# Kernel optimization log

Measured on AMD Instinct MI355X. Metric: run time of the kernel, lower is better.

Reference implementation:

```python
import jax, jax.numpy as jnp
import numpy as np

N = 16
FS = 48000
NFFT = FS * 8            # irfft length hard-coded in the module
F = NFFT // 2 + 1        # 192001 frequency sample points
DELAYS = [809, 877, 937, 1049, 1151, 1249, 1373, 1499,
          1617, 1753, 1879, 2003, 2131, 2269, 2393, 2521]
GAIN_PER_SAMPLE = 0.9998


def setup_inputs() -> dict:
    key = jax.random.key(0)
    k1, k2, k3 = jax.random.split(key, 3)
    # frequency sample points on the upper half of the unit circle (rfft bins)
    omega = jnp.linspace(0.0, np.pi, F).astype(jnp.float32)
    x_real = jnp.cos(omega)
    x_imag = jnp.sin(omega)
    B = jax.random.normal(k1, (1, N, 1), dtype=jnp.float32) / N
    C = jax.random.normal(k2, (1, 1, N), dtype=jnp.float32) / N
    X = jax.random.normal(k3, (N, N), dtype=jnp.float32)  # raw Linear weight (pre-parametrization)
    return {"x_real": x_real, "x_imag": x_imag, "B": B, "C": C, "X": X}


def _delays_m():
    # torch does (m - mean)/std then forward undoes it: m = m_norm*std + mean
    m = jnp.asarray(DELAYS, dtype=jnp.float32)
    mStd = jnp.std(m, ddof=1)   # torch.std is unbiased
    mAvr = jnp.mean(m)
    m_norm = (m - mAvr) / mStd
    return m_norm * mStd + mAvr


def reference(x_real, x_imag, B, C, X):
    x = (x_real + 1j * x_imag).astype(jnp.complex64)          # [F]
    # Skew -> matrix_exp parametrization: A = expm(triu(X,1) - triu(X,1)^T), orthogonal
    Au = jnp.triu(X, 1)
    A = jax.scipy.linalg.expm(Au - Au.T)                       # [N, N]
    m = _delays_m()                                            # [N] float delays
    gamma = jnp.asarray(GAIN_PER_SAMPLE, jnp.float32) ** m     # diag of Gamma, [N]
    AG = (A * gamma[None, :]).astype(jnp.complex64)            # A @ diag(gamma), [N, N]
    # D = diag_embed(x[:,None] ** m) ; build (D - A Gamma) fused
    Dd = x[:, None] ** m[None, :]                              # [F, N] complex
    M = Dd[:, :, None] * jnp.eye(N, dtype=jnp.complex64) - AG[None, :, :]  # [F, N, N]
    Bc = B.astype(jnp.complex64)                               # [1, N, 1], broadcasts over F
    Hch = jnp.linalg.solve(M, Bc)                              # [F, N, 1]  == inv(M) @ B
    H = Hch[:, :, 0] * C.astype(jnp.complex64).reshape(1, N)   # [F, N]
    Hs = jnp.sum(H, axis=-1)                                   # [F]
    mask = jnp.where(x == 0, 0.0, 1.0).astype(jnp.complex64)   # H_mask zeroing x==0 bins
    h = jnp.fft.irfft(Hs * mask, n=NFFT)                       # [NFFT] real
    h = h / jnp.max(jnp.abs(h))
    return H, h
```

## Files before the change

### kernel.cpp

```cpp
#include <hip/hip_runtime.h>
#include <math.h>

#define NN 16
#define FF 192001
#define NFFTN 384000
#define N1F 1024
#define N2F 375
#define TWO_PI 6.283185307179586476925286766559

__constant__ float c_delays[16] = {809.f, 877.f, 937.f, 1049.f, 1151.f, 1249.f, 1373.f, 1499.f,
                                   1617.f, 1753.f, 1879.f, 2003.f, 2131.f, 2269.f, 2393.f, 2521.f};
__constant__ int c_idelays[16] = {809, 877, 937, 1049, 1151, 1249, 1373, 1499,
                                  1617, 1753, 1879, 2003, 2131, 2269, 2393, 2521};

typedef float v2f __attribute__((ext_vector_type(2)));

__device__ __forceinline__ float fastrcp(float x) {
#if __has_builtin(__builtin_amdgcn_rcpf)
  return __builtin_amdgcn_rcpf(x);
#else
  return 1.0f / x;
#endif
}

__global__ void expm_kernel(const float* __restrict__ X, float* __restrict__ AGout,
                            unsigned* __restrict__ mx) {
  if (threadIdx.x == 0) *mx = 0u;
  __shared__ double S[16][16], P[16][16], E[16][16];
  const int i = threadIdx.x >> 4, j = threadIdx.x & 15;
  double xu = (j > i) ? (double)X[i * 16 + j] : 0.0;
  double xl = (i > j) ? (double)X[j * 16 + i] : 0.0;
  double s = (xu - xl) * (1.0 / 256.0);
  S[i][j] = s;
  P[i][j] = s;
  E[i][j] = (i == j ? 1.0 : 0.0) + s;
  __syncthreads();
  for (int k = 2; k <= 24; ++k) {
    double acc = 0.0;
#pragma unroll
    for (int l = 0; l < 16; ++l) acc += P[i][l] * S[l][j];
    acc /= (double)k;
    __syncthreads();
    P[i][j] = acc;
    E[i][j] += acc;
    __syncthreads();
  }
  for (int t = 0; t < 8; ++t) {
    double acc = 0.0;
#pragma unroll
    for (int l = 0; l < 16; ++l) acc += E[i][l] * E[l][j];
    __syncthreads();
    E[i][j] = acc;
    __syncthreads();
  }
  double g = exp((double)c_delays[j] * log(0.9998));
  AGout[i * 16 + j] = (float)(E[i][j] * g);
}

template <int S>
__device__ __forceinline__ v2f bc8(v2f v) {
  v2f o;
  o[0] = __int_as_float(__builtin_amdgcn_ds_swizzle(__float_as_int(v[0]), (S << 5) | 0x18));
  o[1] = __int_as_float(__builtin_amdgcn_ds_swizzle(__float_as_int(v[1]), (S << 5) | 0x18));
  return o;
}

template <int K, int C>
struct ColLoop {
  static __device__ __forceinline__ void run(v2f (&A)[17], v2f (&B)[17],
                                             v2f nA0, v2f A1, v2f nB0, v2f B1) {
    v2f pc;
    if constexpr (K & 1) pc = bc8<(K >> 1)>(B[C]);
    else                 pc = bc8<(K >> 1)>(A[C]);
    v2f pcs = {pc[1], pc[0]};
    A[C] = __builtin_elementwise_fma(nA0, pc, A[C]);
    A[C] = __builtin_elementwise_fma(A1, pcs, A[C]);
    B[C] = __builtin_elementwise_fma(nB0, pc, B[C]);
    B[C] = __builtin_elementwise_fma(B1, pcs, B[C]);
    ColLoop<K, C + 1>::run(A, B, nA0, A1, nB0, B1);
  }
};
template <int K>
struct ColLoop<K, 17> {
  static __device__ __forceinline__ void run(v2f (&)[17], v2f (&)[17], v2f, v2f, v2f, v2f) {}
};

template <int K>
struct GJStep8 {
  static __device__ __forceinline__ void run(v2f (&A)[17], v2f (&B)[17], int s) {
    constexpr int S = K >> 1;
    v2f pk;
    if constexpr (K & 1) pk = bc8<S>(B[K]);
    else                 pk = bc8<S>(A[K]);
    float invd = fastrcp(pk[0] * pk[0] + pk[1] * pk[1]);
    float rcx = pk[0] * invd, rcy = -pk[1] * invd;
    bool ispA, ispB;
    if constexpr (K & 1) { ispA = false; ispB = (s == S); }
    else                 { ispA = (s == S); ispB = false; }
    v2f mA = A[K], mB = B[K];
    float frAx = ispA ? (1.0f - rcx) : (mA[0] * rcx - mA[1] * rcy);
    float frAy = ispA ? (-rcy)       : (mA[0] * rcy + mA[1] * rcx);
    float frBx = ispB ? (1.0f - rcx) : (mB[0] * rcx - mB[1] * rcy);
    float frBy = ispB ? (-rcy)       : (mB[0] * rcy + mB[1] * rcx);
    v2f nA0 = {-frAx, -frAx}, A1 = {frAy, -frAy};
    v2f nB0 = {-frBx, -frBx}, B1 = {frBy, -frBy};
    ColLoop<K, K + 1>::run(A, B, nA0, A1, nB0, B1);
    GJStep8<K + 1>::run(A, B, s);
  }
};
template <>
struct GJStep8<16> {
  static __device__ __forceinline__ void run(v2f (&)[17], v2f (&)[17], int) {}
};

template <bool CPLX>
__global__ __launch_bounds__(256, 4) void solve_kernel(
    const float* __restrict__ Bv, const float* __restrict__ Cv,
    const float* __restrict__ AGin, float* __restrict__ Hout,
    float2* __restrict__ G) {
  __shared__ float AGp[16][17];
  __shared__ float Bs[16], Cs[16];
  const int tid = threadIdx.x;
  AGp[tid >> 4][tid & 15] = AGin[tid];
  if (tid < 16) { Bs[tid] = Bv[tid]; Cs[tid] = Cv[tid]; }
  const int s = tid & 7;
  const int a = 2 * s, b = a + 1;
  int f = blockIdx.x * 32 + (tid >> 3);
  const bool active = (f < FF);
  if (!active) f = FF - 1;
  __syncthreads();

  int pa = (c_idelays[a] * f) % NFFTN;
  int pb = (c_idelays[b] * f) % NFFTN;
  float tha = (float)pa * (float)(TWO_PI / (double)NFFTN);
  float thb = (float)pb * (float)(TWO_PI / (double)NFFTN);
  float sa, ca, sb, cb;
  sincosf(tha, &sa, &ca);
  sincosf(thb, &sb, &cb);

  v2f A[17], B[17];
#pragma unroll
  for (int c = 0; c < 16; ++c) {
    float reA = -AGp[a][c], imA = 0.0f;
    float reB = -AGp[b][c], imB = 0.0f;
    if ((c & 1) == 0) {
      if (c == a) { reA += ca; imA = sa; }
    } else {
      if (c == b) { reB += cb; imB = sb; }
    }
    A[c] = (v2f){reA, imA};
    B[c] = (v2f){reB, imB};
  }
  A[16] = (v2f){Bs[a], 0.0f};
  B[16] = (v2f){Bs[b], 0.0f};

  GJStep8<0>::run(A, B, s);

  const float cca = Cs[a], ccb = Cs[b];
  v2f hA = {A[16][0] * cca, A[16][1] * cca};
  v2f hB = {B[16][0] * ccb, B[16][1] * ccb};
  if (active) {
    if (CPLX) {
      ((float2*)Hout)[(size_t)f * 16 + a] = make_float2(hA[0], hA[1]);
      ((float2*)Hout)[(size_t)f * 16 + b] = make_float2(hB[0], hB[1]);
    } else {
      *(float2*)&Hout[(size_t)f * 16 + a] = make_float2(hA[0], hB[0]);
    }
  }
  float sx = hA[0] + hB[0], sy = hA[1] + hB[1];
#pragma unroll
  for (int off = 4; off > 0; off >>= 1) {
    sx += __shfl_xor(sx, off, 8);
    sy += __shfl_xor(sy, off, 8);
  }
  if (active && s == 0) {
    if (f == 0 || f == 192000) sy = 0.0f;
    G[f] = make_float2(sx, sy);
    if (f > 0 && f < 192000) G[NFFTN - f] = make_float2(sx, -sy);
  }
}

__global__ __launch_bounds__(256) void fftA_kernel(const float2* __restrict__ G,
                                                   float2* __restrict__ Bb) {
  __shared__ float2 buf[2][1024];
  const int k2 = blockIdx.x;
  const int tid = threadIdx.x;
#pragma unroll
  for (int rr = 0; rr < 4; ++rr) {
    int k1 = tid + 256 * rr;
    buf[0][k1] = G[k2 + 375 * k1];
  }
  __syncthreads();
  int src = 0, nt = 1024, s = 1;
  for (int st = 0; st < 10; ++st) {
    int m = nt >> 1;
#pragma unroll
    for (int rr = 0; rr < 2; ++rr) {
      int jj = tid + 256 * rr;
      int p = jj >> st;
      int q = jj & (s - 1);
      float ang = (float)p * (6.28318530717958647692f / (float)nt);
      float ws_, wc_;
      sincosf(ang, &ws_, &wc_);
      float2 a = buf[src][q + s * p];
      float2 b = buf[src][q + s * (p + m)];
      float2 sum = make_float2(a.x + b.x, a.y + b.y);
      float2 d = make_float2(a.x - b.x, a.y - b.y);
      float2 wd = make_float2(d.x * wc_ - d.y * ws_, d.x * ws_ + d.y * wc_);
      buf[src ^ 1][q + s * (2 * p)] = sum;
      buf[src ^ 1][q + s * (2 * p + 1)] = wd;
    }
    __syncthreads();
    src ^= 1;
    nt >>= 1;
    s <<= 1;
  }
  const double tw0 = TWO_PI * (double)k2 / (double)NFFTN;
#pragma unroll
  for (int rr = 0; rr < 4; ++rr) {
    int t1 = tid + 256 * rr;
    float2 vz = buf[src][t1];
    float a = (float)(tw0 * (double)t1);
    float sn, cs;
    sincosf(a, &sn, &cs);
    Bb[t1 * 375 + k2] = make_float2(vz.x * cs - vz.y * sn, vz.x * sn + vz.y * cs);
  }
}

__global__ __launch_bounds__(384) void fftB_kernel(const float2* __restrict__ Bb,
                                                   float* __restrict__ hout,
                                                   unsigned* __restrict__ mx) {
  __shared__ float2 bv[375];
  __shared__ float2 tw[375];
  __shared__ float2 Y[375];
  __shared__ float wmax[6];
  const int t1 = blockIdx.x;
  const int tid = threadIdx.x;
  if (tid < 375) {
    bv[tid] = Bb[t1 * 375 + tid];
    float ang = (float)(TWO_PI * (double)tid / 375.0);
    float s, c;
    sincosf(ang, &s, &c);
    tw[tid] = make_float2(c, s);
  }
  __syncthreads();
  if (tid < 375) {
    const int a = tid / 15, u = tid - 15 * a;
    float ax = 0.f, ay = 0.f;
    int i15 = 0;
#pragma unroll
    for (int b = 0; b < 15; ++b) {
      float2 x = bv[a + 25 * b];
      float2 w = tw[i15 * 25];
      ax += x.x * w.x - x.y * w.y;
      ay += x.x * w.y + x.y * w.x;
      i15 += u;
      if (i15 >= 15) i15 -= 15;
    }
    Y[tid] = make_float2(ax, ay);
  }
  __syncthreads();
  float m = 0.0f;
  if (tid < 375) {
    const int t = tid;
    const int u = t % 15;
    float acc = 0.f;
    int idx = 0;
#pragma unroll
    for (int a = 0; a < 25; ++a) {
      float2 y = Y[a * 15 + u];
      float2 w = tw[idx];
      acc += y.x * w.x - y.y * w.y;
      idx += t;
      if (idx >= 375) idx -= 375;
    }
    float hv = acc * (1.0f / (float)NFFTN);
    hout[t1 + 1024 * t] = hv;
    m = fabsf(hv);
  }
#pragma unroll
  for (int off = 32; off > 0; off >>= 1) m = fmaxf(m, __shfl_xor(m, off, 64));
  if ((tid & 63) == 0) wmax[tid >> 6] = m;
  __syncthreads();
  if (tid == 0) {
    float mm = wmax[0];
#pragma unroll
    for (int w = 1; w < 6; ++w) mm = fmaxf(mm, wmax[w]);
    atomicMax(mx, __float_as_uint(mm));
  }
}

__global__ void norm_kernel(float* __restrict__ h, const unsigned* __restrict__ mx) {
  int i = blockIdx.x * blockDim.x + threadIdx.x;
  float mv = __uint_as_float(*mx);
  if (i < NFFTN) h[i] = h[i] / mv;
}

extern "C" void kernel_launch(void* const* d_in, const int* in_sizes, int n_in,
                              void* d_out, int out_size, void* d_ws, size_t ws_size,
                              hipStream_t stream) {
  (void)in_sizes; (void)n_in; (void)ws_size;
  const float* Bv = (const float*)d_in[2];
  const float* Cv = (const float*)d_in[3];
  const float* X  = (const float*)d_in[4];
  float* out = (float*)d_out;
  char* ws = (char*)d_ws;
  float2* G    = (float2*)(ws);
  float2* Bb   = (float2*)(ws + 3072000);
  unsigned* mx = (unsigned*)(ws + 6144000);
  float*  AGw  = (float*)(ws + 6144064);

  float* htail = out + (out_size - NFFTN);

  expm_kernel<<<1, 256, 0, stream>>>(X, AGw, mx);
  if (out_size >= 2 * FF * NN + NFFTN) {
    solve_kernel<true><<<(FF + 31) / 32, 256, 0, stream>>>(Bv, Cv, AGw, out, G);
  } else {
    solve_kernel<false><<<(FF + 31) / 32, 256, 0, stream>>>(Bv, Cv, AGw, out, G);
  }
  fftA_kernel<<<N2F, 256, 0, stream>>>(G, Bb);
  fftB_kernel<<<N1F, 384, 0, stream>>>(Bb, htail, mx);
  norm_kernel<<<1500, 256, 0, stream>>>(htail, mx);
}
```

Baseline: 166.1 us.

## Solve with 4 rows per thread and transpose-staged FFT with twiddle tables

Each frequency's 16x16 Gauss-Jordan solve now runs on 4 lanes, each holding 4 rows, instead of 8 lanes with 2 rows each. This cuts swizzle broadcasts per FMA and allows vectorised float4 stores of H, at the cost of more registers (launch bounds lowered to 2 blocks). The FFT stage adds two tiled transpose kernels so the 1024-point column FFT reads and writes contiguously instead of striding by 375. Per-butterfly sincosf calls are replaced by shared twiddle tables and a factorised final twiddle. The extra kernels add launches and memory round trips.

```diff
diff --git a/kernel.cpp b/kernel.cpp
--- a/kernel.cpp
+++ b/kernel.cpp
@@ -21,6 +21,10 @@
 #else
   return 1.0f / x;
 #endif
+}
+
+__device__ __forceinline__ float2 cmulf(float2 a, float2 b) {
+  return make_float2(a.x * b.x - a.y * b.y, a.x * b.y + a.y * b.x);
 }
 
 __global__ void expm_kernel(const float* __restrict__ X, float* __restrict__ AGout,
@@ -58,121 +62,158 @@
 }
 
 template <int S>
-__device__ __forceinline__ v2f bc8(v2f v) {
+__device__ __forceinline__ v2f bc4(v2f v) {
   v2f o;
-  o[0] = __int_as_float(__builtin_amdgcn_ds_swizzle(__float_as_int(v[0]), (S << 5) | 0x18));
-  o[1] = __int_as_float(__builtin_amdgcn_ds_swizzle(__float_as_int(v[1]), (S << 5) | 0x18));
+  o[0] = __int_as_float(__builtin_amdgcn_ds_swizzle(__float_as_int(v[0]), (S << 5) | 0x1C));
+  o[1] = __int_as_float(__builtin_amdgcn_ds_swizzle(__float_as_int(v[1]), (S << 5) | 0x1C));
   return o;
 }
 
 template <int K, int C>
-struct ColLoop {
-  static __device__ __forceinline__ void run(v2f (&A)[17], v2f (&B)[17],
-                                             v2f nA0, v2f A1, v2f nB0, v2f B1) {
+struct ColLoop4 {
+  static __device__ __forceinline__ void run(
+      v2f (&M0)[17], v2f (&M1)[17], v2f (&M2)[17], v2f (&M3)[17],
+      v2f f0a, v2f f0b, v2f f1a, v2f f1b, v2f f2a, v2f f2b, v2f f3a, v2f f3b) {
+    constexpr int SL = K & 3, S = K >> 2;
     v2f pc;
-    if constexpr (K & 1) pc = bc8<(K >> 1)>(B[C]);
-    else                 pc = bc8<(K >> 1)>(A[C]);
+    if constexpr (SL == 0) pc = bc4<S>(M0[C]);
+    else if constexpr (SL == 1) pc = bc4<S>(M1[C]);
+    else if constexpr (SL == 2) pc = bc4<S>(M2[C]);
+    else pc = bc4<S>(M3[C]);
     v2f pcs = {pc[1], pc[0]};
-    A[C] = __builtin_elementwise_fma(nA0, pc, A[C]);
-    A[C] = __builtin_elementwise_fma(A1, pcs, A[C]);
-    B[C] = __builtin_elementwise_fma(nB0, pc, B[C]);
-    B[C] = __builtin_elementwise_fma(B1, pcs, B[C]);
-    ColLoop<K, C + 1>::run(A, B, nA0, A1, nB0, B1);
+    M0[C] = __builtin_elementwise_fma(f0a, pc, M0[C]);
+    M0[C] = __builtin_elementwise_fma(f0b, pcs, M0[C]);
+    M1[C] = __builtin_elementwise_fma(f1a, pc, M1[C]);
+    M1[C] = __builtin_elementwise_fma(f1b, pcs, M1[C]);
+    M2[C] = __builtin_elementwise_fma(f2a, pc, M2[C]);
+    M2[C] = __builtin_elementwise_fma(f2b, pcs, M2[C]);
+    M3[C] = __builtin_elementwise_fma(f3a, pc, M3[C]);
+    M3[C] = __builtin_elementwise_fma(f3b, pcs, M3[C]);
+    ColLoop4<K, C + 1>::run(M0, M1, M2, M3, f0a, f0b, f1a, f1b, f2a, f2b, f3a, f3b);
   }
 };
 template <int K>
-struct ColLoop<K, 17> {
-  static __device__ __forceinline__ void run(v2f (&)[17], v2f (&)[17], v2f, v2f, v2f, v2f) {}
+struct ColLoop4<K, 17> {
+  static __device__ __forceinline__ void run(v2f (&)[17], v2f (&)[17], v2f (&)[17], v2f (&)[17],
+                                             v2f, v2f, v2f, v2f, v2f, v2f, v2f, v2f) {}
 };
 
 template <int K>
-struct GJStep8 {
-  static __device__ __forceinline__ void run(v2f (&A)[17], v2f (&B)[17], int s) {
-    constexpr int S = K >> 1;
+struct GJStep4 {
+  static __device__ __forceinline__ void run(v2f (&M0)[17], v2f (&M1)[17], v2f (&M2)[17],
+                                             v2f (&M3)[17], int s) {
+    constexpr int SL = K & 3, S = K >> 2;
     v2f pk;
-    if constexpr (K & 1) pk = bc8<S>(B[K]);
-    else                 pk = bc8<S>(A[K]);
+    if constexpr (SL == 0) pk = bc4<S>(M0[K]);
+    else if constexpr (SL == 1) pk = bc4<S>(M1[K]);
+    else if constexpr (SL == 2) pk = bc4<S>(M2[K]);
+    else pk = bc4<S>(M3[K]);
     float invd = fastrcp(pk[0] * pk[0] + pk[1] * pk[1]);
     float rcx = pk[0] * invd, rcy = -pk[1] * invd;
-    bool ispA, ispB;
-    if constexpr (K & 1) { ispA = false; ispB = (s == S); }
-    else                 { ispA = (s == S); ispB = false; }
-    v2f mA = A[K], mB = B[K];
-    float frAx = ispA ? (1.0f - rcx) : (mA[0] * rcx - mA[1] * rcy);
-    float frAy = ispA ? (-rcy)       : (mA[0] * rcy + mA[1] * rcx);
-    float frBx = ispB ? (1.0f - rcx) : (mB[0] * rcx - mB[1] * rcy);
-    float frBy = ispB ? (-rcy)       : (mB[0] * rcy + mB[1] * rcx);
-    v2f nA0 = {-frAx, -frAx}, A1 = {frAy, -frAy};
-    v2f nB0 = {-frBx, -frBx}, B1 = {frBy, -frBy};
-    ColLoop<K, K + 1>::run(A, B, nA0, A1, nB0, B1);
-    GJStep8<K + 1>::run(A, B, s);
+    const bool inS = (s == S);
+    v2f m0 = M0[K], m1 = M1[K], m2 = M2[K], m3 = M3[K];
+    const bool p0 = inS && (SL == 0), p1 = inS && (SL == 1);
+    const bool p2 = inS && (SL == 2), p3 = inS && (SL == 3);
+    float f0x = p0 ? (1.0f - rcx) : (m0[0] * rcx - m0[1] * rcy);
+    float f0y = p0 ? (-rcy)       : (m0[0] * rcy + m0[1] * rcx);
+    float f1x = p1 ? (1.0f - rcx) : (m1[0] * rcx - m1[1] * rcy);
+    float f1y = p1 ? (-rcy)       : (m1[0] * rcy + m1[1] * rcx);
+    float f2x = p2 ? (1.0f - rcx) : (m2[0] * rcx - m2[1] * rcy);
+    float f2y = p2 ? (-rcy)       : (m2[0] * rcy + m2[1] * rcx);
+    float f3x = p3 ? (1.0f - rcx) : (m3[0] * rcx - m3[1] * rcy);
+    float f3y = p3 ? (-rcy)       : (m3[0] * rcy + m3[1] * rcx);
+    ColLoop4<K, K + 1>::run(M0, M1, M2, M3,
+                            (v2f){-f0x, -f0x}, (v2f){f0y, -f0y},
+                            (v2f){-f1x, -f1x}, (v2f){f1y, -f1y},
+                            (v2f){-f2x, -f2x}, (v2f){f2y, -f2y},
+                            (v2f){-f3x, -f3x}, (v2f){f3y, -f3y});
+    GJStep4<K + 1>::run(M0, M1, M2, M3, s);
   }
 };
 template <>
-struct GJStep8<16> {
-  static __device__ __forceinline__ void run(v2f (&)[17], v2f (&)[17], int) {}
+struct GJStep4<16> {
+  static __device__ __forceinline__ void run(v2f (&)[17], v2f (&)[17], v2f (&)[17], v2f (&)[17], int) {}
 };
 
+#define INITROW(Mj, jj, cj, sj)                                                   \
+  do {                                                                            \
+    const int rr_ = a0 + jj;                                                      \
+    float4 q0 = AG4[rr_ * 4 + 0], q1 = AG4[rr_ * 4 + 1];                          \
+    float4 q2 = AG4[rr_ * 4 + 2], q3 = AG4[rr_ * 4 + 3];                          \
+    Mj[0]  = (v2f){(rr_ == 0  ? cj : 0.0f) - q0.x, (rr_ == 0  ? sj : 0.0f)};      \
+    Mj[1]  = (v2f){(rr_ == 1  ? cj : 0.0f) - q0.y, (rr_ == 1  ? sj : 0.0f)};      \
+    Mj[2]  = (v2f){(rr_ == 2  ? cj : 0.0f) - q0.z, (rr_ == 2  ? sj : 0.0f)};      \
+    Mj[3]  = (v2f){(rr_ == 3  ? cj : 0.0f) - q0.w, (rr_ == 3  ? sj : 0.0f)};      \
+    Mj[4]  = (v2f){(rr_ == 4  ? cj : 0.0f) - q1.x, (rr_ == 4  ? sj : 0.0f)};      \
+    Mj[5]  = (v2f){(rr_ == 5  ? cj : 0.0f) - q1.y, (rr_ == 5  ? sj : 0.0f)};      \
+    Mj[6]  = (v2f){(rr_ == 6  ? cj : 0.0f) - q1.z, (rr_ == 6  ? sj : 0.0f)};      \
+    Mj[7]  = (v2f){(rr_ == 7  ? cj : 0.0f) - q1.w, (rr_ == 7  ? sj : 0.0f)};      \
+    Mj[8]  = (v2f){(rr_ == 8  ? cj : 0.0f) - q2.x, (rr_ == 8  ? sj : 0.0f)};      \
+    Mj[9]  = (v2f){(rr_ == 9  ? cj : 0.0f) - q2.y, (rr_ == 9  ? sj : 0.0f)};      \
+    Mj[10] = (v2f){(rr_ == 10 ? cj : 0.0f) - q2.z, (rr_ == 10 ? sj : 0.0f)};      \
+    Mj[11] = (v2f){(rr_ == 11 ? cj : 0.0f) - q2.w, (rr_ == 11 ? sj : 0.0f)};      \
+    Mj[12] = (v2f){(rr_ == 12 ? cj : 0.0f) - q3.x, (rr_ == 12 ? sj : 0.0f)};      \
+    Mj[13] = (v2f){(rr_ == 13 ? cj : 0.0f) - q3.y, (rr_ == 13 ? sj : 0.0f)};      \
+    Mj[14] = (v2f){(rr_ == 14 ? cj : 0.0f) - q3.z, (rr_ == 14 ? sj : 0.0f)};      \
+    Mj[15] = (v2f){(rr_ == 15 ? cj : 0.0f) - q3.w, (rr_ == 15 ? sj : 0.0f)};      \
+    Mj[16] = (v2f){Bs[rr_], 0.0f};                                                \
+  } while (0)
+
 template <bool CPLX>
-__global__ __launch_bounds__(256, 4) void solve_kernel(
+__global__ __launch_bounds__(256, 2) void solve_kernel(
     const float* __restrict__ Bv, const float* __restrict__ Cv,
     const float* __restrict__ AGin, float* __restrict__ Hout,
     float2* __restrict__ G) {
-  __shared__ float AGp[16][17];
+  __shared__ float AGs[16][16];
   __shared__ float Bs[16], Cs[16];
   const int tid = threadIdx.x;
-  AGp[tid >> 4][tid & 15] = AGin[tid];
+  AGs[tid >> 4][tid & 15] = AGin[tid];
   if (tid < 16) { Bs[tid] = Bv[tid]; Cs[tid] = Cv[tid]; }
-  const int s = tid & 7;
-  const int a = 2 * s, b = a + 1;
-  int f = blockIdx.x * 32 + (tid >> 3);
+  const int s = tid & 3;
+  const int a0 = s << 2;
+  int f = blockIdx.x * 64 + (tid >> 2);
   const bool active = (f < FF);
   if (!active) f = FF - 1;
   __syncthreads();
 
-  int pa = (c_idelays[a] * f) % NFFTN;
-  int pb = (c_idelays[b] * f) % NFFTN;
-  float tha = (float)pa * (float)(TWO_PI / (double)NFFTN);
-  float thb = (float)pb * (float)(TWO_PI / (double)NFFTN);
-  float sa, ca, sb, cb;
-  sincosf(tha, &sa, &ca);
-  sincosf(thb, &sb, &cb);
-
-  v2f A[17], B[17];
-#pragma unroll
-  for (int c = 0; c < 16; ++c) {
-    float reA = -AGp[a][c], imA = 0.0f;
-    float reB = -AGp[b][c], imB = 0.0f;
-    if ((c & 1) == 0) {
-      if (c == a) { reA += ca; imA = sa; }
-    } else {
-      if (c == b) { reB += cb; imB = sb; }
-    }
-    A[c] = (v2f){reA, imA};
-    B[c] = (v2f){reB, imB};
-  }
-  A[16] = (v2f){Bs[a], 0.0f};
-  B[16] = (v2f){Bs[b], 0.0f};
-
-  GJStep8<0>::run(A, B, s);
-
-  const float cca = Cs[a], ccb = Cs[b];
-  v2f hA = {A[16][0] * cca, A[16][1] * cca};
-  v2f hB = {B[16][0] * ccb, B[16][1] * ccb};
+  int ph0 = (c_idelays[a0 + 0] * f) % NFFTN;
+  int ph1 = (c_idelays[a0 + 1] * f) % NFFTN;
+  int ph2 = (c_idelays[a0 + 2] * f) % NFFTN;
+  int ph3 = (c_idelays[a0 + 3] * f) % NFFTN;
+  const float k2r = (float)(TWO_PI / (double)NFFTN);
+  float c0, s0, c1, s1, c2, s2, c3, s3;
+  sincosf((float)ph0 * k2r, &s0, &c0);
+  sincosf((float)ph1 * k2r, &s1, &c1);
+  sincosf((float)ph2 * k2r, &s2, &c2);
+  sincosf((float)ph3 * k2r, &s3, &c3);
+
+  const float4* AG4 = (const float4*)&AGs[0][0];
+  v2f M0[17], M1[17], M2[17], M3[17];
+  INITROW(M0, 0, c0, s0);
+  INITROW(M1, 1, c1, s1);
+  INITROW(M2, 2, c2, s2);
+  INITROW(M3, 3, c3, s3);
+
+  GJStep4<0>::run(M0, M1, M2, M3, s);
+
+  const float cc0 = Cs[a0 + 0], cc1 = Cs[a0 + 1], cc2 = Cs[a0 + 2], cc3 = Cs[a0 + 3];
+  v2f h0 = {M0[16][0] * cc0, M0[16][1] * cc0};
+  v2f h1 = {M1[16][0] * cc1, M1[16][1] * cc1};
+  v2f h2 = {M2[16][0] * cc2, M2[16][1] * cc2};
+  v2f h3 = {M3[16][0] * cc3, M3[16][1] * cc3};
   if (active) {
     if (CPLX) {
-      ((float2*)Hout)[(size_t)f * 16 + a] = make_float2(hA[0], hA[1]);
-      ((float2*)Hout)[(size_t)f * 16 + b] = make_float2(hB[0], hB[1]);
+      float4* dst = (float4*)((float2*)Hout + (size_t)f * 16 + a0);
+      dst[0] = (float4){h0[0], h0[1], h1[0], h1[1]};
+      dst[1] = (float4){h2[0], h2[1], h3[0], h3[1]};
     } else {
-      *(float2*)&Hout[(size_t)f * 16 + a] = make_float2(hA[0], hB[0]);
+      *(float4*)&Hout[(size_t)f * 16 + a0] = (float4){h0[0], h1[0], h2[0], h3[0]};
     }
   }
-  float sx = hA[0] + hB[0], sy = hA[1] + hB[1];
-#pragma unroll
-  for (int off = 4; off > 0; off >>= 1) {
-    sx += __shfl_xor(sx, off, 8);
-    sy += __shfl_xor(sy, off, 8);
-  }
+  float sx = h0[0] + h1[0] + h2[0] + h3[0];
+  float sy = h0[1] + h1[1] + h2[1] + h3[1];
+  sx += __shfl_xor(sx, 1, 4); sy += __shfl_xor(sy, 1, 4);
+  sx += __shfl_xor(sx, 2, 4); sy += __shfl_xor(sy, 2, 4);
   if (active && s == 0) {
     if (f == 0 || f == 192000) sy = 0.0f;
     G[f] = make_float2(sx, sy);
@@ -180,50 +221,106 @@
   }
 }
 
-__global__ __launch_bounds__(256) void fftA_kernel(const float2* __restrict__ G,
-                                                   float2* __restrict__ Bb) {
+__global__ __launch_bounds__(256) void t1_kernel(const float2* __restrict__ G,
+                                                 float2* __restrict__ GT) {
+  __shared__ float2 tile[32][33];
+  const int k1b = blockIdx.x * 32, k2b = blockIdx.y * 32;
+  const int tx = threadIdx.x & 31, ty = threadIdx.x >> 5;
+#pragma unroll
+  for (int i = 0; i < 4; ++i) {
+    int k1 = k1b + ty + 8 * i;
+    int k2 = k2b + tx;
+    if (k2 < N2F) tile[ty + 8 * i][tx] = G[k2 + N2F * k1];
+  }
+  __syncthreads();
+#pragma unroll
+  for (int i = 0; i < 4; ++i) {
+    int k2 = k2b + ty + 8 * i;
+    int k1 = k1b + tx;
+    if (k2 < N2F) GT[k2 * 1024 + k1] = tile[tx][ty + 8 * i];
+  }
+}
+
+__global__ __launch_bounds__(256) void fftA_kernel(const float2* __restrict__ GT,
+                                                   float2* __restrict__ AT) {
   __shared__ float2 buf[2][1024];
+  __shared__ float2 wtab[512];
+  __shared__ float2 wA[32], wB[32];
   const int k2 = blockIdx.x;
   const int tid = threadIdx.x;
 #pragma unroll
   for (int rr = 0; rr < 4; ++rr) {
     int k1 = tid + 256 * rr;
-    buf[0][k1] = G[k2 + 375 * k1];
-  }
-  __syncthreads();
-  int src = 0, nt = 1024, s = 1;
+    buf[0][k1] = GT[k2 * 1024 + k1];
+  }
+  {
+    float s_, c_;
+    sincosf((float)tid * (float)(TWO_PI / 1024.0), &s_, &c_);
+    wtab[tid] = make_float2(c_, s_);
+    sincosf((float)(tid + 256) * (float)(TWO_PI / 1024.0), &s_, &c_);
+    wtab[tid + 256] = make_float2(c_, s_);
+  }
+  if (tid < 64) {
+    double base = TWO_PI * (double)k2 / (double)NFFTN;
+    float s_, c_;
+    if (tid < 32) {
+      sincosf((float)(base * (double)tid), &s_, &c_);
+      wA[tid] = make_float2(c_, s_);
+    } else {
+      int j = tid - 32;
+      sincosf((float)(base * 32.0 * (double)j), &s_, &c_);
+      wB[j] = make_float2(c_, s_);
+    }
+  }
+  __syncthreads();
+  int src = 0;
+#pragma unroll
   for (int st = 0; st < 10; ++st) {
-    int m = nt >> 1;
-#pragma unroll
-    for (int rr = 0; rr < 2; ++rr) {
-      int jj = tid + 256 * rr;
+    const int sS = 1 << st;
+    const int m = 512 >> st;
+#pragma unroll
+    for (int rr2 = 0; rr2 < 2; ++rr2) {
+      int jj = tid + 256 * rr2;
       int p = jj >> st;
-      int q = jj & (s - 1);
-      float ang = (float)p * (6.28318530717958647692f / (float)nt);
-      float ws_, wc_;
-      sincosf(ang, &ws_, &wc_);
-      float2 a = buf[src][q + s * p];
-      float2 b = buf[src][q + s * (p + m)];
+      int q = jj & (sS - 1);
+      float2 w = wtab[p << st];
+      float2 a = buf[src][q + sS * p];
+      float2 b = buf[src][q + sS * (p + m)];
       float2 sum = make_float2(a.x + b.x, a.y + b.y);
       float2 d = make_float2(a.x - b.x, a.y - b.y);
-      float2 wd = make_float2(d.x * wc_ - d.y * ws_, d.x * ws_ + d.y * wc_);
-      buf[src ^ 1][q + s * (2 * p)] = sum;
-      buf[src ^ 1][q + s * (2 * p + 1)] = wd;
+      float2 wd = make_float2(d.x * w.x - d.y * w.y, d.x * w.y + d.y * w.x);
+      buf[src ^ 1][q + sS * (2 * p)] = sum;
+      buf[src ^ 1][q + sS * (2 * p + 1)] = wd;
     }
     __syncthreads();
     src ^= 1;
-    nt >>= 1;
-    s <<= 1;
-  }
-  const double tw0 = TWO_PI * (double)k2 / (double)NFFTN;
+  }
 #pragma unroll
   for (int rr = 0; rr < 4; ++rr) {
     int t1 = tid + 256 * rr;
     float2 vz = buf[src][t1];
-    float a = (float)(tw0 * (double)t1);
-    float sn, cs;
-    sincosf(a, &sn, &cs);
-    Bb[t1 * 375 + k2] = make_float2(vz.x * cs - vz.y * sn, vz.x * sn + vz.y * cs);
+    float2 tw = cmulf(wA[t1 & 31], wB[t1 >> 5]);
+    AT[k2 * 1024 + t1] = cmulf(vz, tw);
+  }
+}
+
+__global__ __launch_bounds__(256) void t2_kernel(const float2* __restrict__ AT,
+                                                 float2* __restrict__ Bb) {
+  __shared__ float2 tile[32][33];
+  const int t1b = blockIdx.x * 32, k2b = blockIdx.y * 32;
+  const int tx = threadIdx.x & 31, ty = threadIdx.x >> 5;
+#pragma unroll
+  for (int i = 0; i < 4; ++i) {
+    int k2 = k2b + ty + 8 * i;
+    int t1 = t1b + tx;
+    if (k2 < N2F) tile[ty + 8 * i][tx] = AT[k2 * 1024 + t1];
+  }
+  __syncthreads();
+#pragma unroll
+  for (int i = 0; i < 4; ++i) {
+    int t1 = t1b + ty + 8 * i;
+    int k2 = k2b + tx;
+    if (k2 < N2F) Bb[t1 * N2F + k2] = tile[tx][ty + 8 * i];
   }
 }
 
@@ -237,7 +334,7 @@
   const int t1 = blockIdx.x;
   const int tid = threadIdx.x;
   if (tid < 375) {
-    bv[tid] = Bb[t1 * 375 + tid];
+    bv[tid] = Bb[t1 * N2F + tid];
     float ang = (float)(TWO_PI * (double)tid / 375.0);
     float s, c;
     sincosf(ang, &s, &c);
@@ -305,8 +402,8 @@
   const float* X  = (const float*)d_in[4];
   float* out = (float*)d_out;
   char* ws = (char*)d_ws;
-  float2* G    = (float2*)(ws);
-  float2* Bb   = (float2*)(ws + 3072000);
+  float2* buf0 = (float2*)(ws);
+  float2* buf1 = (float2*)(ws + 3072000);
   unsigned* mx = (unsigned*)(ws + 6144000);
   float*  AGw  = (float*)(ws + 6144064);
 
@@ -314,11 +411,13 @@
 
   expm_kernel<<<1, 256, 0, stream>>>(X, AGw, mx);
   if (out_size >= 2 * FF * NN + NFFTN) {
-    solve_kernel<true><<<(FF + 31) / 32, 256, 0, stream>>>(Bv, Cv, AGw, out, G);
+    solve_kernel<true><<<(FF + 63) / 64, 256, 0, stream>>>(Bv, Cv, AGw, out, buf0);
   } else {
-    solve_kernel<false><<<(FF + 31) / 32, 256, 0, stream>>>(Bv, Cv, AGw, out, G);
-  }
-  fftA_kernel<<<N2F, 256, 0, stream>>>(G, Bb);
-  fftB_kernel<<<N1F, 384, 0, stream>>>(Bb, htail, mx);
+    solve_kernel<false><<<(FF + 63) / 64, 256, 0, stream>>>(Bv, Cv, AGw, out, buf0);
+  }
+  t1_kernel<<<dim3(32, 12), 256, 0, stream>>>(buf0, buf1);
+  fftA_kernel<<<N2F, 256, 0, stream>>>(buf1, buf0);
+  t2_kernel<<<dim3(32, 12), 256, 0, stream>>>(buf0, buf1);
+  fftB_kernel<<<N1F, 384, 0, stream>>>(buf1, htail, mx);
   norm_kernel<<<1500, 256, 0, stream>>>(htail, mx);
 }
```

Measured after the change: 155.7 us. 6.3% less time.
